# Optimization experiments

Hardware: AMD Instinct MI355X
Metric: run time of the kernel (lower is better)

Reference implementation:

```python
import jax, jax.numpy as jnp
import numpy as np

N, D, H, E, K = 16384, 1024, 4096, 8, 2
PROJ = min(D // 2, 256)  # 256
CLAMP_MAX = float(np.log(1.0 / 0.01))  # log(100)


def setup_inputs() -> dict:
    key = jax.random.key(0)
    ks = jax.random.split(key, 10)
    x = jax.random.normal(ks[0], (N, D), dtype=jnp.float32)
    # cosine gate params
    Wp = jax.random.normal(ks[1], (D, PROJ), dtype=jnp.float32) * (1.0 / np.sqrt(D))
    bp = jnp.zeros((PROJ,), dtype=jnp.float32)
    sim = jax.random.normal(ks[2], (PROJ, E), dtype=jnp.float32) * 0.01
    temp = jnp.full((1,), float(np.log(1.0 / 0.5)), dtype=jnp.float32)  # log(1/init_t)
    # expert FFN params (mmcv FFN: linear->GELU->linear, add_identity)
    W1 = jax.random.normal(ks[3], (E, D, H), dtype=jnp.float32) * (1.0 / np.sqrt(D))
    b1 = jnp.zeros((E, H), dtype=jnp.float32)
    W2 = jax.random.normal(ks[4], (E, H, D), dtype=jnp.float32) * (1.0 / np.sqrt(H))
    b2 = jnp.zeros((E, D), dtype=jnp.float32)
    return {"x": x, "Wp": Wp, "bp": bp, "sim": sim, "temp": temp,
            "W1": W1, "b1": b1, "W2": W2, "b2": b2}


def _l2norm(v, axis):
    # F.normalize: v / max(||v||, 1e-12)
    n = jnp.sqrt(jnp.sum(v * v, axis=axis, keepdims=True))
    return v / jnp.maximum(n, 1e-12)


def _gates(x, Wp, bp, sim, temp):
    proj = _l2norm(x @ Wp + bp, axis=1)          # [N, PROJ], row-normalized
    logits = proj @ _l2norm(sim, axis=0)          # [N, E] cosine similarities
    scale = jnp.exp(jnp.minimum(temp, CLAMP_MAX))
    logits = logits * scale
    top_v, top_i = jax.lax.top_k(logits, K)       # [N, K]
    top_g = jax.nn.softmax(top_v, axis=-1)        # softmax over top-k logits
    gates = jnp.zeros((x.shape[0], E), dtype=logits.dtype)
    gates = gates.at[jnp.arange(x.shape[0])[:, None], top_i].set(top_g)
    return gates


def reference(x, Wp, bp, sim, temp, W1, b1, W2, b2):
    gates = _gates(x, Wp, bp, sim, temp)          # [N, E], sparse (k nonzeros/row)
    # dispatch + per-expert FFN (add_identity) + gate-weighted combine.
    # gate==0 for non-selected experts, so masked dense accumulation matches
    # the sort/split/index_add combine exactly.
    out = jnp.zeros_like(x)
    for e in range(E):
        g = gates[:, e:e + 1]                      # [N, 1]
        h = jax.nn.gelu(x @ W1[e] + b1[e], approximate=False)
        f = h @ W2[e] + b2[e]
        out = out + g * (x + f)                    # FFN residual, gate multiply
    return out
```

## Files before the change

### kernel.cpp

```cpp
#include <hip/hip_runtime.h>
#include <hip/hip_bf16.h>
#include <math.h>

#define N_TOK 16384
#define DIM   1024
#define HID   4096
#define NEXP  8
#define NPROJ 256
#define CLAMP_MAXD 4.605170185988091
#define CLAMP_MAXF 4.605170185988091f
#define TAU 3e-4f

#define MAX_TILES 264
#define MAX_ROWS (MAX_TILES*128)
#define CHUNK_TILES 66
#define NCHUNK 4
#define CHUNK_ROWS (CHUNK_TILES*128)

#define M_CNT   0
#define M_CUR   8
#define M_ROWST 16
#define M_TILEST 25
#define M_TOT   34
#define M_RED   35

typedef __bf16 bf16x8 __attribute__((ext_vector_type(8)));
typedef float  floatx4 __attribute__((ext_vector_type(4)));

__device__ __forceinline__ unsigned short f2bfbits(float f) {
  __hip_bfloat16 b = __float2bfloat16(f);
  union { __hip_bfloat16 b; unsigned short u; } c; c.b = b; return c.u;
}
__device__ __forceinline__ float bf2f(unsigned short u) {
  union { unsigned int u; float f; } c; c.u = ((unsigned int)u) << 16; return c.f;
}
__device__ __forceinline__ float gelu_exact(float z) {
  return 0.5f * z * (1.0f + erff(z * 0.70710678118654752f));
}

__device__ __forceinline__ void gld16(void* lds, const void* g) {
  __builtin_amdgcn_global_load_lds(
      (const __attribute__((address_space(1))) void*)g,
      (__attribute__((address_space(3))) void*)lds, 16, 0, 0);
}


__global__ void k_zero_meta(int* meta) { meta[threadIdx.x] = 0; }

__global__ __launch_bounds__(256) void k_simn(const float* __restrict__ sim,
                                              double* __restrict__ simn,
                                              float* __restrict__ simnf) {
  __shared__ double norms[NEXP];
  int t = threadIdx.x;
  if (t < NEXP) {
    double s = 0.0;
    for (int j = 0; j < NPROJ; ++j) { double v = (double)sim[j*NEXP + t]; s += v*v; }
    double n = sqrt(s); norms[t] = (n > 1e-12 ? n : 1e-12);
  }
  __syncthreads();
  for (int q = 0; q < (NPROJ*NEXP)/256; ++q) {
    int idx = t + q*256; int e = idx & (NEXP-1);
    double v = (double)sim[idx] / norms[e];
    simn[idx] = v; simnf[idx] = (float)v;
  }
}

__global__ __launch_bounds__(256) void k_transpose(const float* __restrict__ in,
                                                   unsigned short* __restrict__ out,
                                                   int R, int C) {
  __shared__ float tile[32][33];
  size_t zoff = (size_t)blockIdx.z * (size_t)R * (size_t)C;
  in += zoff; out += zoff;
  int c  = blockIdx.x*32 + threadIdx.x;
  int r0 = blockIdx.y*32 + threadIdx.y;
  #pragma unroll
  for (int i = 0; i < 4; ++i)
    tile[threadIdx.y + i*8][threadIdx.x] = in[(size_t)(r0 + i*8)*C + c];
  __syncthreads();
  int r  = blockIdx.y*32 + threadIdx.x;
  int c0 = blockIdx.x*32 + threadIdx.y;
  #pragma unroll
  for (int i = 0; i < 4; ++i)
    out[(size_t)(c0 + i*8)*R + r] = f2bfbits(tile[threadIdx.x][threadIdx.y + i*8]);
}

#define GT1 16
__global__ __launch_bounds__(256) void k_gating1(const float* __restrict__ x,
    const float* __restrict__ Wp, const float* __restrict__ bp,
    const float* __restrict__ simnf, const float* __restrict__ temp,
    float* __restrict__ gates, int* __restrict__ eidx, int* __restrict__ meta,
    int* __restrict__ redoList, unsigned short* __restrict__ xbf) {
  __shared__ int hist[NEXP];
  int tid = threadIdx.x, lane = tid & 63;
  int tg = __builtin_amdgcn_readfirstlane(tid >> 6);
  int i0 = blockIdx.x * GT1;
  if (tid < NEXP) hist[tid] = 0;
  {
    const float4* src = (const float4*)(x + (size_t)i0*DIM);
    ushort4* dst = (ushort4*)(xbf + (size_t)i0*DIM);
    #pragma unroll
    for (int q = 0; q < GT1*DIM/4/256; ++q) {
      float4 v = src[tid + q*256];
      ushort4 o; o.x=f2bfbits(v.x); o.y=f2bfbits(v.y); o.z=f2bfbits(v.z); o.w=f2bfbits(v.w);
      dst[tid + q*256] = o;
    }
  }
  __syncthreads();
  const float* xr0 = x + (size_t)(i0 + tg*4 + 0)*DIM;
  const float* xr1 = x + (size_t)(i0 + tg*4 + 1)*DIM;
  const float* xr2 = x + (size_t)(i0 + tg*4 + 2)*DIM;
  const float* xr3 = x + (size_t)(i0 + tg*4 + 3)*DIM;
  float acc[4][4];
  #pragma unroll
  for (int t = 0; t < 4; ++t)
    #pragma unroll
    for (int q = 0; q < 4; ++q) acc[t][q] = 0.f;
  for (int d = 0; d < DIM; d += 4) {
    float4 xv[4];
    xv[0] = *(const float4*)&xr0[d]; xv[1] = *(const float4*)&xr1[d];
    xv[2] = *(const float4*)&xr2[d]; xv[3] = *(const float4*)&xr3[d];
    #pragma unroll
    for (int dd = 0; dd < 4; ++dd) {
      float4 wv = *(const float4*)&Wp[(size_t)(d+dd)*NPROJ + 4*lane];
      #pragma unroll
      for (int t = 0; t < 4; ++t) {
        float xs = ((const float*)&xv[t])[dd];
        acc[t][0] += xs*wv.x; acc[t][1] += xs*wv.y;
        acc[t][2] += xs*wv.z; acc[t][3] += xs*wv.w;
      }
    }
  }
  float4 bpv = *(const float4*)&bp[4*lane];
  float sn[4][8];
  #pragma unroll
  for (int q = 0; q < 4; ++q) {
    float4 a = *(const float4*)&simnf[(4*lane+q)*NEXP];
    float4 b = *(const float4*)&simnf[(4*lane+q)*NEXP + 4];
    sn[q][0]=a.x; sn[q][1]=a.y; sn[q][2]=a.z; sn[q][3]=a.w;
    sn[q][4]=b.x; sn[q][5]=b.y; sn[q][6]=b.z; sn[q][7]=b.w;
  }
  float tp = fminf(temp[0], CLAMP_MAXF);
  float esc = expf(tp);
  #pragma unroll
  for (int t = 0; t < 4; ++t) {
    float v[4];
    v[0]=acc[t][0]+bpv.x; v[1]=acc[t][1]+bpv.y; v[2]=acc[t][2]+bpv.z; v[3]=acc[t][3]+bpv.w;
    float vals[9];
    vals[0] = v[0]*v[0] + v[1]*v[1] + v[2]*v[2] + v[3]*v[3];
    #pragma unroll
    for (int e = 0; e < NEXP; ++e)
      vals[1+e] = v[0]*sn[0][e] + v[1]*sn[1][e] + v[2]*sn[2][e] + v[3]*sn[3][e];
    #pragma unroll
    for (int off = 32; off > 0; off >>= 1)
      #pragma unroll
      for (int k = 0; k < 9; ++k) vals[k] += __shfl_xor(vals[k], off, 64);
    float den = sqrtf(vals[0]); den = fmaxf(den, 1e-12f);
    float l[8];
    #pragma unroll
    for (int e = 0; e < NEXP; ++e) l[e] = vals[1+e] / den;
    int iA = 0; float vA = l[0];
    #pragma unroll
    for (int e = 1; e < NEXP; ++e) if (l[e] > vA) { vA = l[e]; iA = e; }
    int iB = -1; float vB = -1e30f;
    #pragma unroll
    for (int e = 0; e < NEXP; ++e) if (e != iA && l[e] > vB) { vB = l[e]; iB = e; }
    float vC = -1e30f;
    #pragma unroll
    for (int e = 0; e < NEXP; ++e) if (e != iA && e != iB && l[e] > vC) vC = l[e];
    if (lane == 0) {
      int i = i0 + tg*4 + t;
      if (vB - vC < TAU) {
        int p = atomicAdd(&meta[M_RED], 1);
        redoList[p] = i;
      } else {
        float ex = expf((vB - vA) * esc);
        float g0 = 1.f / (1.f + ex);
        gates[2*i] = g0; gates[2*i+1] = ex / (1.f + ex);
        eidx[2*i] = iA; eidx[2*i+1] = iB;
        atomicAdd(&hist[iA], 1); atomicAdd(&hist[iB], 1);
      }
    }
  }
  __syncthreads();
  if (tid < NEXP && hist[tid] > 0) atomicAdd(&meta[M_CNT + tid], hist[tid]);
}

__global__ __launch_bounds__(256) void k_gredo(const float* __restrict__ x,
    const float* __restrict__ Wp, const float* __restrict__ bp,
    const double* __restrict__ simn, const float* __restrict__ temp,
    float* __restrict__ gates, int* __restrict__ eidx, int* __restrict__ meta,
    const int* __restrict__ redoList) {
  __shared__ double wred[4][9];
  int nredo = meta[M_RED];
  int tid = threadIdx.x, lane = tid & 63, wv = tid >> 6;
  for (int r = blockIdx.x; r < nredo; r += gridDim.x) {
    int i = redoList[r];
    const float* xr = x + (size_t)i*DIM;
    int j = tid;
    double acc = 0.0;
    for (int d = 0; d < DIM; d += 4) {
      float4 xv = *(const float4*)&xr[d];
      acc += (double)xv.x * (double)Wp[(size_t)(d+0)*NPROJ + j];
      acc += (double)xv.y * (double)Wp[(size_t)(d+1)*NPROJ + j];
      acc += (double)xv.z * (double)Wp[(size_t)(d+2)*NPROJ + j];
      acc += (double)xv.w * (double)Wp[(size_t)(d+3)*NPROJ + j];
    }
    double v = acc + (double)bp[j];
    double vals[9];
    vals[0] = v*v;
    #pragma unroll
    for (int e = 0; e < NEXP; ++e) vals[1+e] = v * simn[j*NEXP + e];
    #pragma unroll
    for (int off = 32; off > 0; off >>= 1)
      #pragma unroll
      for (int k = 0; k < 9; ++k) vals[k] += __shfl_xor(vals[k], off, 64);
    if (lane == 0)
      #pragma unroll
      for (int k = 0; k < 9; ++k) wred[wv][k] = vals[k];
    __syncthreads();
    if (tid == 0) {
      double s[9];
      #pragma unroll
      for (int k = 0; k < 9; ++k)
        s[k] = wred[0][k] + wred[1][k] + wred[2][k] + wred[3][k];
      double den = sqrt(s[0]); if (den < 1e-12) den = 1e-12;
      double tp = (double)temp[0]; if (tp > CLAMP_MAXD) tp = CLAMP_MAXD;
      double sc = exp(tp) / den;
      double l[NEXP];
      #pragma unroll
      for (int e = 0; e < NEXP; ++e) l[e] = s[e+1]*sc;
      int iA = 0; double vA = l[0];
      for (int e = 1; e < NEXP; ++e) if (l[e] > vA) { vA = l[e]; iA = e; }
      int iB = -1; double vB = -1e300;
      for (int e = 0; e < NEXP; ++e) if (e != iA && l[e] > vB) { vB = l[e]; iB = e; }
      double ex = exp(vB - vA);
      double g0 = 1.0/(1.0+ex);
      gates[2*i] = (float)g0; gates[2*i+1] = (float)(ex/(1.0+ex));
      eidx[2*i] = iA; eidx[2*i+1] = iB;
      atomicAdd(&meta[M_CNT + iA], 1); atomicAdd(&meta[M_CNT + iB], 1);
    }
    __syncthreads();
  }
}

__global__ void k_offsets(int* meta) {
  int accT = 0;
  for (int e = 0; e < NEXP; ++e) {
    meta[M_TILEST + e] = accT;
    meta[M_ROWST + e]  = accT * 128;
    accT += (meta[M_CNT + e] + 127) >> 7;
  }
  meta[M_TILEST + NEXP] = accT;
  meta[M_ROWST + NEXP]  = accT * 128;
  meta[M_TOT] = accT;
}

__global__ void k_inittok(int* tok) { tok[blockIdx.x*256 + threadIdx.x] = 0; }

__global__ void k_fill(const int* __restrict__ eidx, int* meta,
                       int* __restrict__ tok, int* __restrict__ rowOf) {
  int i = blockIdx.x*256 + threadIdx.x;
  if (i >= N_TOK) return;
  #pragma unroll
  for (int k = 0; k < 2; ++k) {
    int e = eidx[2*i + k];
    int pos = atomicAdd(&meta[M_CUR + e], 1);
    int row = meta[M_ROWST + e] + pos;
    tok[row] = i;
    rowOf[2*i + k] = row;
  }
}

union LdsU {
  struct { short A[2][128*64]; short B[2][128*64]; } s;
  float C[32*132];
};

template<int ACT>
__global__ __launch_bounds__(256) void k_gemm(
    const unsigned short* __restrict__ Abase, const int* __restrict__ rowmap, int aRowOff,
    const unsigned short* __restrict__ Bbase, long bExpStride,
    const float* __restrict__ biasBase, int biasStride,
    unsigned short* __restrict__ Cbase, int ldc, int cRowOff,
    const int* __restrict__ meta, int tileBase, int K) {
  __shared__ LdsU lds;
  int flat = (int)(blockIdx.y * gridDim.x + blockIdx.x);
  int nwg  = (int)(gridDim.x * gridDim.y);
  int q8 = nwg >> 3, r8 = nwg & 7;
  int xcd = flat & 7, sub = flat >> 3;
  int W = (xcd < r8 ? xcd * (q8 + 1) : r8 * (q8 + 1) + (xcd - r8) * q8) + sub;
  int bx = W / CHUNK_TILES;
  int by = W - bx * CHUNK_TILES;
  int rt = tileBase + by;
  if (rt >= meta[M_TOT]) return;
  int e = 0;
  #pragma unroll
  for (int q = 1; q < NEXP; ++q) if (rt >= meta[M_TILEST + q]) e = q;
  const unsigned short* Bexp = Bbase + (size_t)e * (size_t)bExpStride;
  int tid = threadIdx.x;
  int lane = tid & 63, wv = tid >> 6, mw = wv >> 1, nw = wv & 1;
  int ntBase = bx * 128;
  int lr = lane >> 3;
  int sg = lane & 7;
  const unsigned short* aG[4]; const unsigned short* bG[4];
  #pragma unroll
  for (int jj = 0; jj < 4; ++jj) {
    int r = wv*32 + jj*8 + lr;
    int g = sg ^ (r & 7);
    int grow = rt*128 + r;
    int arow = rowmap ? rowmap[grow] : (grow - aRowOff);
    aG[jj] = Abase + (size_t)arow * (size_t)K + g*8;
    bG[jj] = Bexp + (size_t)(ntBase + r) * (size_t)K + g*8;
  }
  floatx4 acc[4][4];
  #pragma unroll
  for (int mi = 0; mi < 4; ++mi)
    #pragma unroll
    for (int ni = 0; ni < 4; ++ni) acc[mi][ni] = (floatx4){0.f,0.f,0.f,0.f};
  const int nK = K >> 6;
  #pragma unroll
  for (int jj = 0; jj < 4; ++jj) {
    gld16(&lds.s.A[0][(wv*32 + jj*8)*64], aG[jj]);
    gld16(&lds.s.B[0][(wv*32 + jj*8)*64], bG[jj]);
  }
  for (int kt = 0; kt < nK; ++kt) {
    int cur = kt & 1;
    if (kt + 1 < nK) {
      int nxt = cur ^ 1;
      #pragma unroll
      for (int jj = 0; jj < 4; ++jj) {
        gld16(&lds.s.A[nxt][(wv*32 + jj*8)*64], aG[jj] + ((kt + 1) << 6));
        gld16(&lds.s.B[nxt][(wv*32 + jj*8)*64], bG[jj] + ((kt + 1) << 6));
      }
      asm volatile("s_waitcnt vmcnt(8)" ::: "memory");
    } else {
      asm volatile("s_waitcnt vmcnt(0)" ::: "memory");
    }
    __builtin_amdgcn_s_barrier();
    const short* As = lds.s.A[cur];
    const short* Bs = lds.s.B[cur];
    #pragma unroll
    for (int ks = 0; ks < 2; ++ks) {
      int gk = ks*4 + (lane >> 4);
      bf16x8 af[4], bfr[4];
      #pragma unroll
      for (int mi = 0; mi < 4; ++mi) {
        int m = mw*64 + mi*16 + (lane & 15);
        af[mi] = *(const bf16x8*)&As[m*64 + (gk ^ (m & 7))*8];
      }
      #pragma unroll
      for (int ni = 0; ni < 4; ++ni) {
        int n = nw*64 + ni*16 + (lane & 15);
        bfr[ni] = *(const bf16x8*)&Bs[n*64 + (gk ^ (n & 7))*8];
      }
      #pragma unroll
      for (int mi = 0; mi < 4; ++mi)
        #pragma unroll
        for (int ni = 0; ni < 4; ++ni)
          acc[mi][ni] = __builtin_amdgcn_mfma_f32_16x16x32_bf16(af[mi], bfr[ni], acc[mi][ni], 0,0,0);
    }
    __builtin_amdgcn_s_barrier();
  }
  const float* bias = biasBase + (size_t)e * (size_t)biasStride + ntBase;
  #pragma unroll
  for (int p = 0; p < 4; ++p) {
    __syncthreads();
    int lrow0 = mw*16 + ((lane>>4)<<2);
    int lcol  = nw*64 + (lane & 15);
    #pragma unroll
    for (int ni = 0; ni < 4; ++ni)
      #pragma unroll
      for (int jj = 0; jj < 4; ++jj)
        lds.C[(lrow0 + jj)*132 + lcol + ni*16] = acc[p][ni][jj];
    __syncthreads();
    #pragma unroll
    for (int q = 0; q < 2; ++q) {
      int lin = tid + q*256;
      int r = lin >> 4, c8 = lin & 15;
      float4 v0 = *(float4*)&lds.C[r*132 + c8*8];
      float4 v1 = *(float4*)&lds.C[r*132 + c8*8 + 4];
      float4 b0 = ((const float4*)bias)[c8*2];
      float4 b1 = ((const float4*)bias)[c8*2 + 1];
      v0.x += b0.x; v0.y += b0.y; v0.z += b0.z; v0.w += b0.w;
      v1.x += b1.x; v1.y += b1.y; v1.z += b1.z; v1.w += b1.w;
      if (ACT == 1) {
        v0.x = gelu_exact(v0.x); v0.y = gelu_exact(v0.y);
        v0.z = gelu_exact(v0.z); v0.w = gelu_exact(v0.w);
        v1.x = gelu_exact(v1.x); v1.y = gelu_exact(v1.y);
        v1.z = gelu_exact(v1.z); v1.w = gelu_exact(v1.w);
      }
      int gm = rt*128 + (r>>4)*64 + p*16 + (r & 15) - cRowOff;
      union { unsigned short u[8]; int4 v; } o;
      o.u[0]=f2bfbits(v0.x); o.u[1]=f2bfbits(v0.y); o.u[2]=f2bfbits(v0.z); o.u[3]=f2bfbits(v0.w);
      o.u[4]=f2bfbits(v1.x); o.u[5]=f2bfbits(v1.y); o.u[6]=f2bfbits(v1.z); o.u[7]=f2bfbits(v1.w);
      *(int4*)&Cbase[(size_t)gm*(size_t)ldc + ntBase + c8*8] = o.v;
    }
  }
}

__global__ __launch_bounds__(256) void k_combine(const float* __restrict__ x,
    const unsigned short* __restrict__ f, const int* __restrict__ rowOf,
    const float* __restrict__ gates, float* __restrict__ out) {
  int i = blockIdx.x, t = threadIdx.x;
  int r0 = rowOf[2*i], r1 = rowOf[2*i+1];
  float g0 = gates[2*i], g1 = gates[2*i+1];
  float4 xv = ((const float4*)(x + (size_t)i*DIM))[t];
  ushort4 a = ((const ushort4*)(f + (size_t)r0*DIM))[t];
  ushort4 b = ((const ushort4*)(f + (size_t)r1*DIM))[t];
  float4 o;
  o.x = xv.x + g0*bf2f(a.x) + g1*bf2f(b.x);
  o.y = xv.y + g0*bf2f(a.y) + g1*bf2f(b.y);
  o.z = xv.z + g0*bf2f(a.z) + g1*bf2f(b.z);
  o.w = xv.w + g0*bf2f(a.w) + g1*bf2f(b.w);
  ((float4*)(out + (size_t)i*DIM))[t] = o;
}

extern "C" void kernel_launch(void* const* d_in, const int* in_sizes, int n_in,
                              void* d_out, int out_size, void* d_ws, size_t ws_size,
                              hipStream_t stream) {
  const float* x    = (const float*)d_in[0];
  const float* Wp   = (const float*)d_in[1];
  const float* bp   = (const float*)d_in[2];
  const float* sim  = (const float*)d_in[3];
  const float* temp = (const float*)d_in[4];
  const float* W1   = (const float*)d_in[5];
  const float* b1   = (const float*)d_in[6];
  const float* W2   = (const float*)d_in[7];
  const float* b2   = (const float*)d_in[8];
  float* out = (float*)d_out;

  char* w = (char*)d_ws;
  auto carve = [&](size_t bytes) { char* p = w; w += (bytes + 255) & ~(size_t)255; return p; };
  int*            meta = (int*)           carve(64*sizeof(int));
  float*          gates= (float*)         carve((size_t)N_TOK*2*4);
  int*            eidx = (int*)           carve((size_t)N_TOK*2*4);
  int*            rowOf= (int*)           carve((size_t)N_TOK*2*4);
  int*            tok  = (int*)           carve((size_t)MAX_ROWS*4);
  int*            redoL= (int*)           carve((size_t)N_TOK*4);
  double*         simn = (double*)        carve((size_t)NPROJ*NEXP*8);
  float*          simnf= (float*)         carve((size_t)NPROJ*NEXP*4);
  unsigned short* xbf  = (unsigned short*)carve((size_t)N_TOK*DIM*2);
  unsigned short* W1t  = (unsigned short*)carve((size_t)NEXP*HID*DIM*2);
  unsigned short* W2t  = (unsigned short*)carve((size_t)NEXP*DIM*HID*2);
  unsigned short* h    = (unsigned short*)carve((size_t)CHUNK_ROWS*HID*2);
  unsigned short* f    = (unsigned short*)carve((size_t)MAX_ROWS*DIM*2);

  hipLaunchKernelGGL(k_zero_meta, dim3(1), dim3(64), 0, stream, meta);
  hipLaunchKernelGGL(k_simn, dim3(1), dim3(256), 0, stream, sim, simn, simnf);
  hipLaunchKernelGGL(k_transpose, dim3(HID/32, DIM/32, NEXP), dim3(32,8), 0, stream, W1, W1t, DIM, HID);
  hipLaunchKernelGGL(k_transpose, dim3(DIM/32, HID/32, NEXP), dim3(32,8), 0, stream, W2, W2t, HID, DIM);
  hipLaunchKernelGGL(k_gating1, dim3(N_TOK/GT1), dim3(256), 0, stream,
                     x, Wp, bp, simnf, temp, gates, eidx, meta, redoL, xbf);
  hipLaunchKernelGGL(k_gredo, dim3(128), dim3(256), 0, stream,
                     x, Wp, bp, simn, temp, gates, eidx, meta, redoL);
  hipLaunchKernelGGL(k_offsets, dim3(1), dim3(1), 0, stream, meta);
  hipLaunchKernelGGL(k_inittok, dim3(MAX_ROWS/256), dim3(256), 0, stream, tok);
  hipLaunchKernelGGL(k_fill, dim3(N_TOK/256), dim3(256), 0, stream, eidx, meta, tok, rowOf);
  for (int c = 0; c < NCHUNK; ++c) {
    hipLaunchKernelGGL((k_gemm<1>), dim3(HID/128, CHUNK_TILES), dim3(256), 0, stream,
        xbf, tok, 0, W1t, (long)HID*DIM, b1, HID,
        h, HID, c*CHUNK_ROWS, meta, c*CHUNK_TILES, DIM);
    hipLaunchKernelGGL((k_gemm<0>), dim3(DIM/128, CHUNK_TILES), dim3(256), 0, stream,
        h, (const int*)nullptr, c*CHUNK_ROWS, W2t, (long)DIM*HID, b2, DIM,
        f, DIM, 0, meta, c*CHUNK_TILES, HID);
  }
  hipLaunchKernelGGL(k_combine, dim3(N_TOK), dim3(256), 0, stream, x, f, rowOf, gates, out);
}
```

Before: 1.742 ms.

## Compute gating projection with bf16 MFMA GEMM and split gate scoring kernel

Replaces the fp32 CUDA-core gating projection (x@Wp) with the existing bf16 MFMA GEMM kernel via a new ACT==2 variant that writes fp32 output. A separate kernel converts x to bf16, another does normalization, cosine logits and top-2 selection per token. The redo threshold is widened because bf16 projection loses precision, so more tokens go through the slower fp64 redo path. It adds extra launches and a transpose of Wp, and proj/WpT alias the h buffer.

```diff
diff --git a/kernel.cpp b/kernel.cpp
--- a/kernel.cpp
+++ b/kernel.cpp
@@ -9,7 +9,7 @@
 #define NPROJ 256
 #define CLAMP_MAXD 4.605170185988091
 #define CLAMP_MAXF 4.605170185988091f
-#define TAU 3e-4f
+#define TAUB 2e-3f
 
 #define MAX_TILES 264
 #define MAX_ROWS (MAX_TILES*128)
@@ -84,101 +84,78 @@
     out[(size_t)(c0 + i*8)*R + r] = f2bfbits(tile[threadIdx.x][threadIdx.y + i*8]);
 }
 
-#define GT1 16
-__global__ __launch_bounds__(256) void k_gating1(const float* __restrict__ x,
-    const float* __restrict__ Wp, const float* __restrict__ bp,
+__global__ __launch_bounds__(256) void k_tobf16(const float* __restrict__ x,
+                                                unsigned short* __restrict__ xbf) {
+  const float4* src = (const float4*)x;
+  ushort4* dst = (ushort4*)xbf;
+  const int n4 = N_TOK*DIM/4;
+  for (int i = blockIdx.x*256 + threadIdx.x; i < n4; i += gridDim.x*256) {
+    float4 v = src[i];
+    ushort4 o; o.x=f2bfbits(v.x); o.y=f2bfbits(v.y); o.z=f2bfbits(v.z); o.w=f2bfbits(v.w);
+    dst[i] = o;
+  }
+}
+
+__global__ __launch_bounds__(256) void k_gate(const float* __restrict__ proj,
     const float* __restrict__ simnf, const float* __restrict__ temp,
     float* __restrict__ gates, int* __restrict__ eidx, int* __restrict__ meta,
-    int* __restrict__ redoList, unsigned short* __restrict__ xbf) {
+    int* __restrict__ redoList) {
+  __shared__ float sn[NPROJ*NEXP];
   __shared__ int hist[NEXP];
-  int tid = threadIdx.x, lane = tid & 63;
-  int tg = __builtin_amdgcn_readfirstlane(tid >> 6);
-  int i0 = blockIdx.x * GT1;
+  int tid = threadIdx.x;
   if (tid < NEXP) hist[tid] = 0;
-  {
-    const float4* src = (const float4*)(x + (size_t)i0*DIM);
-    ushort4* dst = (ushort4*)(xbf + (size_t)i0*DIM);
-    #pragma unroll
-    for (int q = 0; q < GT1*DIM/4/256; ++q) {
-      float4 v = src[tid + q*256];
-      ushort4 o; o.x=f2bfbits(v.x); o.y=f2bfbits(v.y); o.z=f2bfbits(v.z); o.w=f2bfbits(v.w);
-      dst[tid + q*256] = o;
-    }
-  }
+  #pragma unroll
+  for (int q = 0; q < NPROJ*NEXP/256; ++q)
+    sn[tid + q*256] = simnf[tid + q*256];
   __syncthreads();
-  const float* xr0 = x + (size_t)(i0 + tg*4 + 0)*DIM;
-  const float* xr1 = x + (size_t)(i0 + tg*4 + 1)*DIM;
-  const float* xr2 = x + (size_t)(i0 + tg*4 + 2)*DIM;
-  const float* xr3 = x + (size_t)(i0 + tg*4 + 3)*DIM;
-  float acc[4][4];
-  #pragma unroll
-  for (int t = 0; t < 4; ++t)
-    #pragma unroll
-    for (int q = 0; q < 4; ++q) acc[t][q] = 0.f;
-  for (int d = 0; d < DIM; d += 4) {
-    float4 xv[4];
-    xv[0] = *(const float4*)&xr0[d]; xv[1] = *(const float4*)&xr1[d];
-    xv[2] = *(const float4*)&xr2[d]; xv[3] = *(const float4*)&xr3[d];
-    #pragma unroll
-    for (int dd = 0; dd < 4; ++dd) {
-      float4 wv = *(const float4*)&Wp[(size_t)(d+dd)*NPROJ + 4*lane];
-      #pragma unroll
-      for (int t = 0; t < 4; ++t) {
-        float xs = ((const float*)&xv[t])[dd];
-        acc[t][0] += xs*wv.x; acc[t][1] += xs*wv.y;
-        acc[t][2] += xs*wv.z; acc[t][3] += xs*wv.w;
-      }
-    }
-  }
-  float4 bpv = *(const float4*)&bp[4*lane];
-  float sn[4][8];
-  #pragma unroll
-  for (int q = 0; q < 4; ++q) {
-    float4 a = *(const float4*)&simnf[(4*lane+q)*NEXP];
-    float4 b = *(const float4*)&simnf[(4*lane+q)*NEXP + 4];
-    sn[q][0]=a.x; sn[q][1]=a.y; sn[q][2]=a.z; sn[q][3]=a.w;
-    sn[q][4]=b.x; sn[q][5]=b.y; sn[q][6]=b.z; sn[q][7]=b.w;
-  }
-  float tp = fminf(temp[0], CLAMP_MAXF);
-  float esc = expf(tp);
-  #pragma unroll
-  for (int t = 0; t < 4; ++t) {
-    float v[4];
-    v[0]=acc[t][0]+bpv.x; v[1]=acc[t][1]+bpv.y; v[2]=acc[t][2]+bpv.z; v[3]=acc[t][3]+bpv.w;
-    float vals[9];
-    vals[0] = v[0]*v[0] + v[1]*v[1] + v[2]*v[2] + v[3]*v[3];
-    #pragma unroll
-    for (int e = 0; e < NEXP; ++e)
-      vals[1+e] = v[0]*sn[0][e] + v[1]*sn[1][e] + v[2]*sn[2][e] + v[3]*sn[3][e];
-    #pragma unroll
-    for (int off = 32; off > 0; off >>= 1)
-      #pragma unroll
-      for (int k = 0; k < 9; ++k) vals[k] += __shfl_xor(vals[k], off, 64);
-    float den = sqrtf(vals[0]); den = fmaxf(den, 1e-12f);
+  int token = blockIdx.x * 128 + (tid >> 1);
+  int h = tid & 1;
+  const float4* pr = (const float4*)(proj + (size_t)token*NPROJ + h*128);
+  float s2 = 0.f;
+  float lg[8];
+  #pragma unroll
+  for (int e = 0; e < 8; ++e) lg[e] = 0.f;
+  #pragma unroll 4
+  for (int j4 = 0; j4 < 32; ++j4) {
+    float4 p4 = pr[j4];
+    #pragma unroll
+    for (int c = 0; c < 4; ++c) {
+      float p = ((const float*)&p4)[c];
+      s2 += p*p;
+      const float* srow = &sn[(h*128 + j4*4 + c)*NEXP];
+      float4 sa = *(const float4*)srow;
+      float4 sb = *(const float4*)(srow + 4);
+      lg[0] += p*sa.x; lg[1] += p*sa.y; lg[2] += p*sa.z; lg[3] += p*sa.w;
+      lg[4] += p*sb.x; lg[5] += p*sb.y; lg[6] += p*sb.z; lg[7] += p*sb.w;
+    }
+  }
+  s2 += __shfl_xor(s2, 1, 64);
+  #pragma unroll
+  for (int e = 0; e < 8; ++e) lg[e] += __shfl_xor(lg[e], 1, 64);
+  if (h == 0) {
+    float den = sqrtf(s2); den = fmaxf(den, 1e-12f);
     float l[8];
     #pragma unroll
-    for (int e = 0; e < NEXP; ++e) l[e] = vals[1+e] / den;
+    for (int e = 0; e < 8; ++e) l[e] = lg[e] / den;
     int iA = 0; float vA = l[0];
     #pragma unroll
-    for (int e = 1; e < NEXP; ++e) if (l[e] > vA) { vA = l[e]; iA = e; }
+    for (int e = 1; e < 8; ++e) if (l[e] > vA) { vA = l[e]; iA = e; }
     int iB = -1; float vB = -1e30f;
     #pragma unroll
-    for (int e = 0; e < NEXP; ++e) if (e != iA && l[e] > vB) { vB = l[e]; iB = e; }
+    for (int e = 0; e < 8; ++e) if (e != iA && l[e] > vB) { vB = l[e]; iB = e; }
     float vC = -1e30f;
     #pragma unroll
-    for (int e = 0; e < NEXP; ++e) if (e != iA && e != iB && l[e] > vC) vC = l[e];
-    if (lane == 0) {
-      int i = i0 + tg*4 + t;
-      if (vB - vC < TAU) {
-        int p = atomicAdd(&meta[M_RED], 1);
-        redoList[p] = i;
-      } else {
-        float ex = expf((vB - vA) * esc);
-        float g0 = 1.f / (1.f + ex);
-        gates[2*i] = g0; gates[2*i+1] = ex / (1.f + ex);
-        eidx[2*i] = iA; eidx[2*i+1] = iB;
-        atomicAdd(&hist[iA], 1); atomicAdd(&hist[iB], 1);
-      }
+    for (int e = 0; e < 8; ++e) if (e != iA && e != iB && l[e] > vC) vC = l[e];
+    if (vB - vC < TAUB) {
+      int p = atomicAdd(&meta[M_RED], 1);
+      redoList[p] = token;
+    } else {
+      float esc = expf(fminf(temp[0], CLAMP_MAXF));
+      float ex = expf((vB - vA) * esc);
+      float g0 = 1.f / (1.f + ex);
+      gates[2*token] = g0; gates[2*token+1] = ex / (1.f + ex);
+      eidx[2*token] = iA; eidx[2*token+1] = iB;
+      atomicAdd(&hist[iA], 1); atomicAdd(&hist[iB], 1);
     }
   }
   __syncthreads();
@@ -282,20 +259,22 @@
     const unsigned short* __restrict__ Bbase, long bExpStride,
     const float* __restrict__ biasBase, int biasStride,
     unsigned short* __restrict__ Cbase, int ldc, int cRowOff,
-    const int* __restrict__ meta, int tileBase, int K) {
+    const int* __restrict__ meta, int tileBase, int K, int nty) {
   __shared__ LdsU lds;
   int flat = (int)(blockIdx.y * gridDim.x + blockIdx.x);
   int nwg  = (int)(gridDim.x * gridDim.y);
   int q8 = nwg >> 3, r8 = nwg & 7;
   int xcd = flat & 7, sub = flat >> 3;
   int W = (xcd < r8 ? xcd * (q8 + 1) : r8 * (q8 + 1) + (xcd - r8) * q8) + sub;
-  int bx = W / CHUNK_TILES;
-  int by = W - bx * CHUNK_TILES;
+  int bx = W / nty;
+  int by = W - bx * nty;
   int rt = tileBase + by;
-  if (rt >= meta[M_TOT]) return;
   int e = 0;
-  #pragma unroll
-  for (int q = 1; q < NEXP; ++q) if (rt >= meta[M_TILEST + q]) e = q;
+  if (ACT != 2) {
+    if (rt >= meta[M_TOT]) return;
+    #pragma unroll
+    for (int q = 1; q < NEXP; ++q) if (rt >= meta[M_TILEST + q]) e = q;
+  }
   const unsigned short* Bexp = Bbase + (size_t)e * (size_t)bExpStride;
   int tid = threadIdx.x;
   int lane = tid & 63, wv = tid >> 6, mw = wv >> 1, nw = wv & 1;
@@ -390,10 +369,16 @@
         v1.z = gelu_exact(v1.z); v1.w = gelu_exact(v1.w);
       }
       int gm = rt*128 + (r>>4)*64 + p*16 + (r & 15) - cRowOff;
-      union { unsigned short u[8]; int4 v; } o;
-      o.u[0]=f2bfbits(v0.x); o.u[1]=f2bfbits(v0.y); o.u[2]=f2bfbits(v0.z); o.u[3]=f2bfbits(v0.w);
-      o.u[4]=f2bfbits(v1.x); o.u[5]=f2bfbits(v1.y); o.u[6]=f2bfbits(v1.z); o.u[7]=f2bfbits(v1.w);
-      *(int4*)&Cbase[(size_t)gm*(size_t)ldc + ntBase + c8*8] = o.v;
+      if (ACT == 2) {
+        float* Cf = (float*)Cbase;
+        *(float4*)&Cf[(size_t)gm*(size_t)ldc + ntBase + c8*8] = v0;
+        *(float4*)&Cf[(size_t)gm*(size_t)ldc + ntBase + c8*8 + 4] = v1;
+      } else {
+        union { unsigned short u[8]; int4 v; } o;
+        o.u[0]=f2bfbits(v0.x); o.u[1]=f2bfbits(v0.y); o.u[2]=f2bfbits(v0.z); o.u[3]=f2bfbits(v0.w);
+        o.u[4]=f2bfbits(v1.x); o.u[5]=f2bfbits(v1.y); o.u[6]=f2bfbits(v1.z); o.u[7]=f2bfbits(v1.w);
+        *(int4*)&Cbase[(size_t)gm*(size_t)ldc + ntBase + c8*8] = o.v;
+      }
     }
   }
 }
@@ -444,13 +429,20 @@
   unsigned short* W2t  = (unsigned short*)carve((size_t)NEXP*DIM*HID*2);
   unsigned short* h    = (unsigned short*)carve((size_t)CHUNK_ROWS*HID*2);
   unsigned short* f    = (unsigned short*)carve((size_t)MAX_ROWS*DIM*2);
+  float*          proj = (float*)h;
+  unsigned short* WpT  = (unsigned short*)(h + (size_t)N_TOK*NPROJ*2);
 
   hipLaunchKernelGGL(k_zero_meta, dim3(1), dim3(64), 0, stream, meta);
   hipLaunchKernelGGL(k_simn, dim3(1), dim3(256), 0, stream, sim, simn, simnf);
   hipLaunchKernelGGL(k_transpose, dim3(HID/32, DIM/32, NEXP), dim3(32,8), 0, stream, W1, W1t, DIM, HID);
   hipLaunchKernelGGL(k_transpose, dim3(DIM/32, HID/32, NEXP), dim3(32,8), 0, stream, W2, W2t, HID, DIM);
-  hipLaunchKernelGGL(k_gating1, dim3(N_TOK/GT1), dim3(256), 0, stream,
-                     x, Wp, bp, simnf, temp, gates, eidx, meta, redoL, xbf);
+  hipLaunchKernelGGL(k_transpose, dim3(NPROJ/32, DIM/32, 1), dim3(32,8), 0, stream, Wp, WpT, DIM, NPROJ);
+  hipLaunchKernelGGL(k_tobf16, dim3(2048), dim3(256), 0, stream, x, xbf);
+  hipLaunchKernelGGL((k_gemm<2>), dim3(NPROJ/128, N_TOK/128), dim3(256), 0, stream,
+      xbf, (const int*)nullptr, 0, WpT, 0L, bp, 0,
+      (unsigned short*)proj, NPROJ, 0, meta, 0, DIM, N_TOK/128);
+  hipLaunchKernelGGL(k_gate, dim3(N_TOK/128), dim3(256), 0, stream,
+                     proj, simnf, temp, gates, eidx, meta, redoL);
   hipLaunchKernelGGL(k_gredo, dim3(128), dim3(256), 0, stream,
                      x, Wp, bp, simn, temp, gates, eidx, meta, redoL);
   hipLaunchKernelGGL(k_offsets, dim3(1), dim3(1), 0, stream, meta);
@@ -459,10 +451,10 @@
   for (int c = 0; c < NCHUNK; ++c) {
     hipLaunchKernelGGL((k_gemm<1>), dim3(HID/128, CHUNK_TILES), dim3(256), 0, stream,
         xbf, tok, 0, W1t, (long)HID*DIM, b1, HID,
-        h, HID, c*CHUNK_ROWS, meta, c*CHUNK_TILES, DIM);
+        h, HID, c*CHUNK_ROWS, meta, c*CHUNK_TILES, DIM, CHUNK_TILES);
     hipLaunchKernelGGL((k_gemm<0>), dim3(DIM/128, CHUNK_TILES), dim3(256), 0, stream,
         h, (const int*)nullptr, c*CHUNK_ROWS, W2t, (long)DIM*HID, b2, DIM,
-        f, DIM, 0, meta, c*CHUNK_TILES, HID);
+        f, DIM, 0, meta, c*CHUNK_TILES, HID, CHUNK_TILES);
   }
   hipLaunchKernelGGL(k_combine, dim3(N_TOK), dim3(256), 0, stream, x, f, rowOf, gates, out);
 }
```

After: 1.858 ms. +6.6%, slower.
